# Kernel optimization log

Measured on AMD Instinct MI355X. Metric: run time of the kernel, lower is better.

The kernel has to match this reference:

```python
import jax, jax.numpy as jnp
import numpy as np

B, S, E, H = 8, 1024, 1024, 16
D = E // H  # head_dim = hidden_size // num_heads


def setup_inputs() -> dict:
    key = jax.random.key(0)
    ks = jax.random.split(key, 9)
    s = 0.02
    return {
        "h":  jax.random.normal(ks[0], (B, S, E), jnp.float32),
        # per-head projection weights stacked over heads; torch Linear(E, D) -> stored [E, D] (x @ W)
        "Wq": jax.random.normal(ks[1], (H, E, D), jnp.float32) * s,
        "bq": jax.random.normal(ks[2], (H, D), jnp.float32) * s,
        "Wk": jax.random.normal(ks[3], (H, E, D), jnp.float32) * s,
        "bk": jax.random.normal(ks[4], (H, D), jnp.float32) * s,
        "Wv": jax.random.normal(ks[5], (H, E, D), jnp.float32) * s,  # dead weight: original passes h as value
        "bv": jax.random.normal(ks[6], (H, D), jnp.float32) * s,
        "Wo": jax.random.normal(ks[7], (E, E), jnp.float32) * s,
        "bo": jax.random.normal(ks[8], (E,), jnp.float32) * s,
    }


def reference(h, Wq, bq, Wk, bk, Wv, bv, Wo, bo):
    # Batched over all heads at once instead of the original Python loop.
    q = jnp.einsum('bse,hed->bhsd', h, Wq) + bq[None, :, None, :]   # [B,H,S,D]
    k = jnp.einsum('bse,hed->bhsd', h, Wk) + bk[None, :, None, :]   # [B,H,S,D]
    # v is computed in the original module but NOT used (do_attention gets h as value)
    _v = jnp.einsum('bse,hed->bhsd', h, Wv) + bv[None, :, None, :]
    scale = 1.0 / jnp.sqrt(jnp.asarray(D, h.dtype))
    scores = jnp.einsum('bhsd,bhtd->bhst', q, k) * scale            # [B,H,S,T]
    # original: F.softmax(scores, dim=1) on per-head [B,S,T] -> query axis = axis 2 here
    weights = jax.nn.softmax(scores, axis=2)
    ctx = jnp.einsum('bhst,bte->bhse', weights, h)                  # value = h (embed_dim), per original
    # torch.cat over dim=1 of per-head [B,S,E] outputs -> [B, H*S, E]
    x = ctx.reshape(B, H * S, E)
    return x @ Wo + bo
```

## Files before the change

### kernel.cpp

```cpp
#include <hip/hip_runtime.h>

#define B_ 8
#define S_ 1024
#define E_ 1024
#define H_ 16
#define D_ 64

typedef __attribute__((ext_vector_type(8))) __bf16 bf16x8;
typedef __attribute__((ext_vector_type(4))) float f32x4;
typedef __attribute__((ext_vector_type(4))) unsigned short u16x4;
typedef __attribute__((ext_vector_type(8))) unsigned short u16x8;

static __device__ __forceinline__ unsigned short f2bf_hw(float f) {
  union { __bf16 b; unsigned short u; } v;
  v.b = (__bf16)f;
  return v.u;
}

#if __has_builtin(__builtin_amdgcn_exp2f)
#define EXP2(x) __builtin_amdgcn_exp2f(x)
#else
#define EXP2(x) exp2f(x)
#endif
#define SCALE2 0.18033688f

#define MFMA16(a, b, c) __builtin_amdgcn_mfma_f32_16x16x32_bf16((a), (b), (c), 0, 0, 0)

__global__ void cast_f32_bf16_kernel(const float* __restrict__ src,
                                     unsigned short* __restrict__ dst, int n4) {
  int i = blockIdx.x * 256 + threadIdx.x;
  if (i >= n4) return;
  float4 v = reinterpret_cast<const float4*>(src)[i];
  u16x4 o;
  o[0] = f2bf_hw(v.x); o[1] = f2bf_hw(v.y); o[2] = f2bf_hw(v.z); o[3] = f2bf_hw(v.w);
  reinterpret_cast<u16x4*>(dst)[i] = o;
}

__global__ void transpose_cast_kernel(const float* __restrict__ src,
                                      unsigned short* __restrict__ dst,
                                      int rows, int cols) {
  __shared__ unsigned short tile[64][65];
  const float* s = src + (size_t)blockIdx.z * rows * cols;
  unsigned short* d = dst + (size_t)blockIdx.z * rows * cols;
  int rb = blockIdx.y * 64, cb = blockIdx.x * 64;
#pragma unroll
  for (int k = 0; k < 16; k++) {
    int idx = threadIdx.x + 256 * k;
    int r = idx >> 6, c = idx & 63;
    tile[r][c] = f2bf_hw(s[(size_t)(rb + r) * cols + cb + c]);
  }
  __syncthreads();
#pragma unroll
  for (int k = 0; k < 16; k++) {
    int idx = threadIdx.x + 256 * k;
    int r = idx >> 6, c = idx & 63;
    d[(size_t)(cb + r) * rows + rb + c] = tile[c][r];
  }
}

__launch_bounds__(256)
__global__ void gemm_G_kernel(const unsigned short* __restrict__ hb,
                              const unsigned short* __restrict__ WoT,
                              unsigned short* __restrict__ Gt) {
  int mblk = blockIdx.x, nblk = blockIdx.y, b = blockIdx.z;
  const unsigned short* A = hb + (size_t)b * S_ * E_;
  int tid = threadIdx.x, l = tid & 63, w = tid >> 6;
  int ws = w & 1, wc = w >> 1, lr = l & 15, lg = l >> 4;
  f32x4 acc[4][4] = {};
  int ar[4], bc[4];
#pragma unroll
  for (int i = 0; i < 4; i++) ar[i] = mblk * 128 + ws * 64 + i * 16 + lr;
#pragma unroll
  for (int j = 0; j < 4; j++) bc[j] = nblk * 128 + wc * 64 + j * 16 + lr;
  for (int k0 = 0; k0 < E_; k0 += 32) {
    bf16x8 a[4], bb[4];
#pragma unroll
    for (int i = 0; i < 4; i++)
      a[i] = *reinterpret_cast<const bf16x8*>(A + (size_t)ar[i] * E_ + k0 + lg * 8);
#pragma unroll
    for (int j = 0; j < 4; j++)
      bb[j] = *reinterpret_cast<const bf16x8*>(WoT + (size_t)bc[j] * E_ + k0 + lg * 8);
#pragma unroll
    for (int i = 0; i < 4; i++)
#pragma unroll
      for (int j = 0; j < 4; j++)
        acc[i][j] = MFMA16(a[i], bb[j], acc[i][j]);
  }
#pragma unroll
  for (int i = 0; i < 4; i++) {
    int t0 = mblk * 128 + ws * 64 + i * 16 + lg * 4;
#pragma unroll
    for (int j = 0; j < 4; j++) {
      u16x4 p;
#pragma unroll
      for (int r = 0; r < 4; r++) p[r] = f2bf_hw(acc[i][j][r]);
      int e = bc[j];
      size_t addr = (((size_t)b * 4 + (e >> 8)) * 32 + (t0 >> 5)) * 8192 +
                    (size_t)(e & 255) * 32 + (t0 & 31);
      *reinterpret_cast<u16x4*>(Gt + addr) = p;
    }
  }
}

__launch_bounds__(256)
__global__ void proj_qk_kernel(const unsigned short* __restrict__ hb,
                               const unsigned short* __restrict__ WqT,
                               const unsigned short* __restrict__ WkT,
                               const float* __restrict__ bq,
                               const float* __restrict__ bk,
                               unsigned short* __restrict__ Qb,
                               unsigned short* __restrict__ Kb) {
  int sblk = blockIdx.x, z = blockIdx.y;
  int b = z >> 4, h = z & 15;
  const unsigned short* A = hb + (size_t)b * S_ * E_;
  const unsigned short* Btq = WqT + (size_t)h * D_ * E_;
  const unsigned short* Btk = WkT + (size_t)h * D_ * E_;
  int tid = threadIdx.x, l = tid & 63, w = tid >> 6;
  int ws = w & 1, wc = w >> 1, lr = l & 15, lg = l >> 4;
  f32x4 accq[4][2] = {}, acck[4][2] = {};
  int ar[4], bc[2];
#pragma unroll
  for (int i = 0; i < 4; i++) ar[i] = sblk * 128 + ws * 64 + i * 16 + lr;
#pragma unroll
  for (int j = 0; j < 2; j++) bc[j] = wc * 32 + j * 16 + lr;
  for (int k0 = 0; k0 < E_; k0 += 32) {
    bf16x8 a[4], bbq[2], bbk[2];
#pragma unroll
    for (int i = 0; i < 4; i++)
      a[i] = *reinterpret_cast<const bf16x8*>(A + (size_t)ar[i] * E_ + k0 + lg * 8);
#pragma unroll
    for (int j = 0; j < 2; j++) {
      bbq[j] = *reinterpret_cast<const bf16x8*>(Btq + (size_t)bc[j] * E_ + k0 + lg * 8);
      bbk[j] = *reinterpret_cast<const bf16x8*>(Btk + (size_t)bc[j] * E_ + k0 + lg * 8);
    }
#pragma unroll
    for (int i = 0; i < 4; i++)
#pragma unroll
      for (int j = 0; j < 2; j++) {
        accq[i][j] = MFMA16(a[i], bbq[j], accq[i][j]);
        acck[i][j] = MFMA16(a[i], bbk[j], acck[i][j]);
      }
  }
  unsigned short* oq = Qb + (size_t)z * S_ * D_;
  unsigned short* ok = Kb + (size_t)z * S_ * D_;
#pragma unroll
  for (int j = 0; j < 2; j++) {
    float bvq = bq[h * D_ + bc[j]], bvk = bk[h * D_ + bc[j]];
#pragma unroll
    for (int i = 0; i < 4; i++)
#pragma unroll
      for (int r = 0; r < 4; r++) {
        int s = sblk * 128 + ws * 64 + i * 16 + lg * 4 + r;
        oq[(size_t)s * D_ + bc[j]] = f2bf_hw(accq[i][j][r] + bvq);
        ok[(size_t)s * D_ + bc[j]] = f2bf_hw(acck[i][j][r] + bvk);
      }
  }
}

__launch_bounds__(256)
__global__ void stats_kernel(const unsigned short* __restrict__ Qb,
                             const unsigned short* __restrict__ Kb,
                             float* __restrict__ c) {
  int tblk = blockIdx.x, z = blockIdx.y;
  const unsigned short* Q = Qb + (size_t)z * S_ * D_;
  const unsigned short* K = Kb + (size_t)z * S_ * D_;
  int tid = threadIdx.x, l = tid & 63, w = tid >> 6;
  int lr = l & 15, lg = l >> 4;
  int tb = tblk * 256 + w * 64;
  const float scale = 0.125f;
  bf16x8 kb[4][2];
#pragma unroll
  for (int j = 0; j < 4; j++)
#pragma unroll
    for (int ks = 0; ks < 2; ks++)
      kb[j][ks] = *reinterpret_cast<const bf16x8*>(
          K + (size_t)(tb + j * 16 + lr) * D_ + ks * 32 + lg * 8);
  float m[4], zz[4];
#pragma unroll
  for (int j = 0; j < 4; j++) { m[j] = -1e30f; zz[j] = 0.f; }
  for (int s0 = 0; s0 < S_; s0 += 32) {
    bf16x8 aq[2][2];
#pragma unroll
    for (int sf = 0; sf < 2; sf++)
#pragma unroll
      for (int ks = 0; ks < 2; ks++)
        aq[sf][ks] = *reinterpret_cast<const bf16x8*>(
            Q + (size_t)(s0 + sf * 16 + lr) * D_ + ks * 32 + lg * 8);
    f32x4 acc[2][4] = {};
#pragma unroll
    for (int sf = 0; sf < 2; sf++)
#pragma unroll
      for (int j = 0; j < 4; j++) {
        acc[sf][j] = MFMA16(aq[sf][0], kb[j][0], acc[sf][j]);
        acc[sf][j] = MFMA16(aq[sf][1], kb[j][1], acc[sf][j]);
      }
#pragma unroll
    for (int j = 0; j < 4; j++) {
      float v[8];
#pragma unroll
      for (int sf = 0; sf < 2; sf++)
#pragma unroll
        for (int r = 0; r < 4; r++) v[sf * 4 + r] = acc[sf][j][r] * scale;
      float mx = m[j];
#pragma unroll
      for (int t = 0; t < 8; t++) mx = fmaxf(mx, v[t]);
      float sum = 0.f;
#pragma unroll
      for (int t = 0; t < 8; t++) sum += __expf(v[t] - mx);
      zz[j] = zz[j] * __expf(m[j] - mx) + sum;
      m[j] = mx;
    }
  }
#pragma unroll
  for (int j = 0; j < 4; j++) {
    float mj = m[j], zj = zz[j];
#pragma unroll
    for (int off = 16; off <= 32; off <<= 1) {
      float om = __shfl_xor(mj, off, 64);
      float oz = __shfl_xor(zj, off, 64);
      float mn = fmaxf(mj, om);
      zj = zj * __expf(mj - mn) + oz * __expf(om - mn);
      mj = mn;
    }
    if (l < 16)
      c[(size_t)z * S_ + tb + j * 16 + lr] = (mj + __logf(zj)) * 1.44269504f;
  }
}

__launch_bounds__(256, 3)
__global__ void attn_kernel(const unsigned short* __restrict__ Qb,
                            const unsigned short* __restrict__ Kb,
                            const unsigned short* __restrict__ Gt,
                            const float* __restrict__ cst,
                            const float* __restrict__ bo,
                            float* __restrict__ out) {
  int n = blockIdx.x;
  int b = n & 7, h = (n >> 3) & 15, eblk = (n >> 7) & 3, sblk = n >> 9;
  int z = b * 16 + h;
  __shared__ unsigned short Ks[2][32][72];
  __shared__ unsigned short Ps[2][64][40];
  int tid = threadIdx.x, l = tid & 63, w = tid >> 6;
  int lr = l & 15, lg = l >> 4;
  const unsigned short* Q = Qb + (size_t)z * S_ * D_ + (size_t)(sblk * 64) * D_;
  const unsigned short* K = Kb + (size_t)z * S_ * D_;
  const unsigned short* Gb = Gt + (((size_t)b * 4 + eblk) * 32) * 8192;
  const float* cz = cst + (size_t)z * S_;

  bf16x8 q[2];
#pragma unroll
  for (int ks = 0; ks < 2; ks++)
    q[ks] = *reinterpret_cast<const bf16x8*>(
        Q + (size_t)(w * 16 + lr) * D_ + ks * 32 + lg * 8);

  size_t goff[4];
#pragma unroll
  for (int j = 0; j < 4; j++)
    goff[j] = (size_t)(w * 64 + j * 16 + lr) * 32 + lg * 8;

  int krow = tid >> 3, kc8 = (tid & 7) * 8;
  u16x8 kreg;
  bf16x8 vA[4], vB[4];

  kreg = *reinterpret_cast<const u16x8*>(K + (size_t)krow * D_ + kc8);
  *reinterpret_cast<u16x8*>(&Ks[0][krow][kc8]) = kreg;
  kreg = *reinterpret_cast<const u16x8*>(K + (size_t)(32 + krow) * D_ + kc8);
#pragma unroll
  for (int j = 0; j < 4; j++)
    vA[j] = *reinterpret_cast<const bf16x8*>(Gb + goff[j]);
  __syncthreads();

  f32x4 acc[4][4] = {};

#define WINDOW(IT, CUR, VPREV, HASPV)                                             \
  do {                                                                            \
    int t0_ = (IT) * 32;                                                          \
                            \
    *reinterpret_cast<u16x8*>(&Ks[(CUR) ^ 1][krow][kc8]) = kreg;                  \
    {                                                                             \
      int tk_ = ((IT) + 2) & 31;                                                  \
      kreg = *reinterpret_cast<const u16x8*>(                                     \
          K + (size_t)(tk_ * 32 + krow) * D_ + kc8);                              \
    }                                                                             \
                                                         \
    f32x4 sa_[2] = {};                                                            \
    {                                                                             \
      bf16x8 ka_[2][2];                                                           \
      _Pragma("unroll") for (int tf = 0; tf < 2; tf++)                            \
        _Pragma("unroll") for (int ks = 0; ks < 2; ks++)                          \
          ka_[tf][ks] = *reinterpret_cast<const bf16x8*>(                         \
              &Ks[CUR][tf * 16 + lr][ks * 32 + lg * 8]);                          \
      _Pragma("unroll") for (int tf = 0; tf < 2; tf++) {                          \
        sa_[tf] = MFMA16(ka_[tf][0], q[0], sa_[tf]);                              \
        sa_[tf] = MFMA16(ka_[tf][1], q[1], sa_[tf]);                              \
      }                                                                           \
    }                                                                             \
                 \
    if (HASPV) {                                                                  \
      bf16x8 ap_[4];                                                              \
      _Pragma("unroll") for (int i = 0; i < 4; i++)                               \
        ap_[i] = *reinterpret_cast<const bf16x8*>(                                \
            &Ps[(CUR) ^ 1][i * 16 + lr][lg * 8]);                                 \
      __builtin_amdgcn_s_setprio(1);                                              \
      _Pragma("unroll") for (int i = 0; i < 4; i++)                               \
        _Pragma("unroll") for (int j = 0; j < 4; j++)                             \
          acc[i][j] = MFMA16(ap_[i], VPREV[j], acc[i][j]);                        \
      __builtin_amdgcn_s_setprio(0);                                              \
    }                                                                             \
           \
    {                                                                             \
      int tg_ = ((IT) + 1) & 31;                                                  \
      _Pragma("unroll") for (int j = 0; j < 4; j++)                               \
        VPREV[j] = *reinterpret_cast<const bf16x8*>(                              \
            Gb + (size_t)tg_ * 8192 + goff[j]);                                   \
    }                                                                             \
                                                         \
    _Pragma("unroll") for (int tf = 0; tf < 2; tf++) {                            \
      f32x4 cv_ = *reinterpret_cast<const f32x4*>(cz + t0_ + tf * 16 + lg * 4);   \
      u16x4 p_;                                                                   \
      _Pragma("unroll") for (int r = 0; r < 4; r++)                               \
        p_[r] = f2bf_hw(EXP2(fmaf(sa_[tf][r], SCALE2, -cv_[r])));                 \
      *reinterpret_cast<u16x4*>(&Ps[CUR][w * 16 + lr][tf * 16 + lg * 4]) = p_;    \
    }                                                                             \
    __syncthreads();                                                              \
  } while (0)

  for (int it2 = 0; it2 < 16; ++it2) {
    WINDOW(it2 * 2, 0, vB, (it2 > 0));
    WINDOW(it2 * 2 + 1, 1, vA, true);
  }
#undef WINDOW

  {
    bf16x8 ap_[4];
#pragma unroll
    for (int i = 0; i < 4; i++)
      ap_[i] = *reinterpret_cast<const bf16x8*>(&Ps[1][i * 16 + lr][lg * 8]);
#pragma unroll
    for (int i = 0; i < 4; i++)
#pragma unroll
      for (int j = 0; j < 4; j++)
        acc[i][j] = MFMA16(ap_[i], vB[j], acc[i][j]);
  }

  float bov[4];
#pragma unroll
  for (int j = 0; j < 4; j++) bov[j] = bo[eblk * 256 + w * 64 + j * 16 + lr];
#pragma unroll
  for (int i = 0; i < 4; i++)
#pragma unroll
    for (int j = 0; j < 4; j++)
#pragma unroll
      for (int r = 0; r < 4; r++) {
        int s = sblk * 64 + i * 16 + lg * 4 + r;
        int col = eblk * 256 + w * 64 + j * 16 + lr;
        out[((size_t)b * (H_ * S_) + (size_t)h * S_ + s) * E_ + col] =
            acc[i][j][r] + bov[j];
      }
}

extern "C" void kernel_launch(void* const* d_in, const int* in_sizes, int n_in,
                              void* d_out, int out_size, void* d_ws, size_t ws_size,
                              hipStream_t stream) {
  const float* h  = (const float*)d_in[0];
  const float* Wq = (const float*)d_in[1];
  const float* bq = (const float*)d_in[2];
  const float* Wk = (const float*)d_in[3];
  const float* bk = (const float*)d_in[4];
  const float* Wo = (const float*)d_in[7];
  const float* bo = (const float*)d_in[8];
  float* out = (float*)d_out;

  char* p = (char*)d_ws;
  unsigned short* hb  = (unsigned short*)p; p += (size_t)B_ * S_ * E_ * 2;
  unsigned short* WoT = (unsigned short*)p; p += (size_t)E_ * E_ * 2;
  unsigned short* WqT = (unsigned short*)p; p += (size_t)H_ * D_ * E_ * 2;
  unsigned short* WkT = (unsigned short*)p; p += (size_t)H_ * D_ * E_ * 2;
  unsigned short* Qb  = (unsigned short*)p; p += (size_t)B_ * H_ * S_ * D_ * 2;
  unsigned short* Kb  = (unsigned short*)p; p += (size_t)B_ * H_ * S_ * D_ * 2;
  unsigned short* Gt  = (unsigned short*)p; p += (size_t)B_ * E_ * S_ * 2;
  float*          cst = (float*)p;          p += (size_t)B_ * H_ * S_ * 4;

  int n4 = B_ * S_ * E_ / 4;
  cast_f32_bf16_kernel<<<dim3(n4 / 256), 256, 0, stream>>>(h, hb, n4);
  transpose_cast_kernel<<<dim3(16, 16, 1), 256, 0, stream>>>(Wo, WoT, E_, E_);
  transpose_cast_kernel<<<dim3(1, 16, H_), 256, 0, stream>>>(Wq, WqT, E_, D_);
  transpose_cast_kernel<<<dim3(1, 16, H_), 256, 0, stream>>>(Wk, WkT, E_, D_);
  gemm_G_kernel<<<dim3(8, 8, B_), 256, 0, stream>>>(hb, WoT, Gt);
  proj_qk_kernel<<<dim3(8, B_ * H_), 256, 0, stream>>>(hb, WqT, WkT, bq, bk, Qb, Kb);
  stats_kernel<<<dim3(S_ / 256, B_ * H_), 256, 0, stream>>>(Qb, Kb, cst);
  attn_kernel<<<dim3(8192), 256, 0, stream>>>(Qb, Kb, Gt, cst, bo, out);
}
```

Measured before the change: 645.4 us.

## Double key tile per window to 64 and stage softmax constants in LDS

Each window of the fused attention+output-projection loop now processes 64 keys instead of 32, so there are half as many windows and half as many block-wide barriers. The V/Gt prefetch is restructured to hold two 32-key slices in registers. The per-row log-sum-exp constants are loaded into shared memory once instead of being read from global memory every window. LDS use and register pressure grow (larger K/P tiles, more live V fragments), which could lower occupancy under the 3-blocks launch bound.

```diff
diff --git a/kernel.cpp b/kernel.cpp
--- a/kernel.cpp
+++ b/kernel.cpp
@@ -237,14 +237,14 @@
   int n = blockIdx.x;
   int b = n & 7, h = (n >> 3) & 15, eblk = (n >> 7) & 3, sblk = n >> 9;
   int z = b * 16 + h;
-  __shared__ unsigned short Ks[2][32][72];
-  __shared__ unsigned short Ps[2][64][40];
+  __shared__ unsigned short Ks[2][64][72];
+  __shared__ unsigned short Ps[2][64][72];
+  __shared__ float csm[1024];
   int tid = threadIdx.x, l = tid & 63, w = tid >> 6;
   int lr = l & 15, lg = l >> 4;
   const unsigned short* Q = Qb + (size_t)z * S_ * D_ + (size_t)(sblk * 64) * D_;
   const unsigned short* K = Kb + (size_t)z * S_ * D_;
   const unsigned short* Gb = Gt + (((size_t)b * 4 + eblk) * 32) * 8192;
-  const float* cz = cst + (size_t)z * S_;
 
   bf16x8 q[2];
 #pragma unroll
@@ -257,65 +257,73 @@
   for (int j = 0; j < 4; j++)
     goff[j] = (size_t)(w * 64 + j * 16 + lr) * 32 + lg * 8;
 
-  int krow = tid >> 3, kc8 = (tid & 7) * 8;
-  u16x8 kreg;
-  bf16x8 vA[4], vB[4];
-
-  kreg = *reinterpret_cast<const u16x8*>(K + (size_t)krow * D_ + kc8);
-  *reinterpret_cast<u16x8*>(&Ks[0][krow][kc8]) = kreg;
-  kreg = *reinterpret_cast<const u16x8*>(K + (size_t)(32 + krow) * D_ + kc8);
-#pragma unroll
-  for (int j = 0; j < 4; j++)
-    vA[j] = *reinterpret_cast<const bf16x8*>(Gb + goff[j]);
+  int krow = tid >> 2, kc16 = (tid & 3) * 16;
+  u16x8 kreg0, kreg1;
+  bf16x8 v[2][4];
+
+  *reinterpret_cast<f32x4*>(&csm[tid * 4]) =
+      *reinterpret_cast<const f32x4*>(cst + (size_t)z * S_ + tid * 4);
+  kreg0 = *reinterpret_cast<const u16x8*>(K + (size_t)krow * D_ + kc16);
+  kreg1 = *reinterpret_cast<const u16x8*>(K + (size_t)krow * D_ + kc16 + 8);
+  *reinterpret_cast<u16x8*>(&Ks[0][krow][kc16]) = kreg0;
+  *reinterpret_cast<u16x8*>(&Ks[0][krow][kc16 + 8]) = kreg1;
+  kreg0 = *reinterpret_cast<const u16x8*>(K + (size_t)(64 + krow) * D_ + kc16);
+  kreg1 = *reinterpret_cast<const u16x8*>(K + (size_t)(64 + krow) * D_ + kc16 + 8);
+#pragma unroll
+  for (int ks = 0; ks < 2; ks++)
+#pragma unroll
+    for (int j = 0; j < 4; j++)
+      v[ks][j] = *reinterpret_cast<const bf16x8*>(Gb + (size_t)ks * 8192 + goff[j]);
   __syncthreads();
 
   f32x4 acc[4][4] = {};
 
-#define WINDOW(IT, CUR, VPREV, HASPV)                                             \
+#define WINDOW(IT, CUR)                                                           \
   do {                                                                            \
-    int t0_ = (IT) * 32;                                                          \
+    int t0_ = (IT) * 64;                                                          \
                             \
-    *reinterpret_cast<u16x8*>(&Ks[(CUR) ^ 1][krow][kc8]) = kreg;                  \
+    *reinterpret_cast<u16x8*>(&Ks[(CUR) ^ 1][krow][kc16]) = kreg0;                \
+    *reinterpret_cast<u16x8*>(&Ks[(CUR) ^ 1][krow][kc16 + 8]) = kreg1;            \
     {                                                                             \
-      int tk_ = ((IT) + 2) & 31;                                                  \
-      kreg = *reinterpret_cast<const u16x8*>(                                     \
-          K + (size_t)(tk_ * 32 + krow) * D_ + kc8);                              \
+      int tk_ = ((IT) + 2) & 15;                                                  \
+      kreg0 = *reinterpret_cast<const u16x8*>(                                    \
+          K + (size_t)(tk_ * 64 + krow) * D_ + kc16);                             \
+      kreg1 = *reinterpret_cast<const u16x8*>(                                    \
+          K + (size_t)(tk_ * 64 + krow) * D_ + kc16 + 8);                         \
     }                                                                             \
-                                                         \
-    f32x4 sa_[2] = {};                                                            \
-    {                                                                             \
-      bf16x8 ka_[2][2];                                                           \
-      _Pragma("unroll") for (int tf = 0; tf < 2; tf++)                            \
-        _Pragma("unroll") for (int ks = 0; ks < 2; ks++)                          \
-          ka_[tf][ks] = *reinterpret_cast<const bf16x8*>(                         \
-              &Ks[CUR][tf * 16 + lr][ks * 32 + lg * 8]);                          \
-      _Pragma("unroll") for (int tf = 0; tf < 2; tf++) {                          \
-        sa_[tf] = MFMA16(ka_[tf][0], q[0], sa_[tf]);                              \
-        sa_[tf] = MFMA16(ka_[tf][1], q[1], sa_[tf]);                              \
+                                            \
+    f32x4 sa_[4];                                                                 \
+    _Pragma("unroll") for (int tf = 0; tf < 4; tf++) {                            \
+      bf16x8 ka0_ = *reinterpret_cast<const bf16x8*>(                             \
+          &Ks[CUR][tf * 16 + lr][lg * 8]);                                        \
+      bf16x8 ka1_ = *reinterpret_cast<const bf16x8*>(                             \
+          &Ks[CUR][tf * 16 + lr][32 + lg * 8]);                                   \
+      f32x4 t_ = {};                                                              \
+      t_ = MFMA16(ka0_, q[0], t_);                                                \
+      sa_[tf] = MFMA16(ka1_, q[1], t_);                                           \
+    }                                                                             \
+               \
+    if ((IT) > 0) {                                                               \
+      __builtin_amdgcn_s_setprio(1);                                              \
+      _Pragma("unroll") for (int ks = 0; ks < 2; ks++) {                          \
+        bf16x8 ap_[4];                                                            \
+        _Pragma("unroll") for (int i = 0; i < 4; i++)                             \
+          ap_[i] = *reinterpret_cast<const bf16x8*>(                              \
+              &Ps[(CUR) ^ 1][i * 16 + lr][ks * 32 + lg * 8]);                     \
+        _Pragma("unroll") for (int i = 0; i < 4; i++)                             \
+          _Pragma("unroll") for (int j = 0; j < 4; j++)                           \
+            acc[i][j] = MFMA16(ap_[i], v[ks][j], acc[i][j]);                      \
       }                                                                           \
+      __builtin_amdgcn_s_setprio(0);                                              \
+                                      \
+      _Pragma("unroll") for (int ks = 0; ks < 2; ks++)                            \
+        _Pragma("unroll") for (int j = 0; j < 4; j++)                             \
+          v[ks][j] = *reinterpret_cast<const bf16x8*>(                            \
+              Gb + ((size_t)(IT) * 2 + ks) * 8192 + goff[j]);                     \
     }                                                                             \
-                 \
-    if (HASPV) {                                                                  \
-      bf16x8 ap_[4];                                                              \
-      _Pragma("unroll") for (int i = 0; i < 4; i++)                               \
-        ap_[i] = *reinterpret_cast<const bf16x8*>(                                \
-            &Ps[(CUR) ^ 1][i * 16 + lr][lg * 8]);                                 \
-      __builtin_amdgcn_s_setprio(1);                                              \
-      _Pragma("unroll") for (int i = 0; i < 4; i++)                               \
-        _Pragma("unroll") for (int j = 0; j < 4; j++)                             \
-          acc[i][j] = MFMA16(ap_[i], VPREV[j], acc[i][j]);                        \
-      __builtin_amdgcn_s_setprio(0);                                              \
-    }                                                                             \
-           \
-    {                                                                             \
-      int tg_ = ((IT) + 1) & 31;                                                  \
-      _Pragma("unroll") for (int j = 0; j < 4; j++)                               \
-        VPREV[j] = *reinterpret_cast<const bf16x8*>(                              \
-            Gb + (size_t)tg_ * 8192 + goff[j]);                                   \
-    }                                                                             \
-                                                         \
-    _Pragma("unroll") for (int tf = 0; tf < 2; tf++) {                            \
-      f32x4 cv_ = *reinterpret_cast<const f32x4*>(cz + t0_ + tf * 16 + lg * 4);   \
+                                 \
+    _Pragma("unroll") for (int tf = 0; tf < 4; tf++) {                            \
+      f32x4 cv_ = *reinterpret_cast<const f32x4*>(&csm[t0_ + tf * 16 + lg * 4]);  \
       u16x4 p_;                                                                   \
       _Pragma("unroll") for (int r = 0; r < 4; r++)                               \
         p_[r] = f2bf_hw(EXP2(fmaf(sa_[tf][r], SCALE2, -cv_[r])));                 \
@@ -324,22 +332,25 @@
     __syncthreads();                                                              \
   } while (0)
 
-  for (int it2 = 0; it2 < 16; ++it2) {
-    WINDOW(it2 * 2, 0, vB, (it2 > 0));
-    WINDOW(it2 * 2 + 1, 1, vA, true);
+  for (int it2 = 0; it2 < 8; ++it2) {
+    WINDOW(it2 * 2, 0);
+    WINDOW(it2 * 2 + 1, 1);
   }
 #undef WINDOW
 
   {
-    bf16x8 ap_[4];
-#pragma unroll
-    for (int i = 0; i < 4; i++)
-      ap_[i] = *reinterpret_cast<const bf16x8*>(&Ps[1][i * 16 + lr][lg * 8]);
-#pragma unroll
-    for (int i = 0; i < 4; i++)
-#pragma unroll
-      for (int j = 0; j < 4; j++)
-        acc[i][j] = MFMA16(ap_[i], vB[j], acc[i][j]);
+#pragma unroll
+    for (int ks = 0; ks < 2; ks++) {
+      bf16x8 ap_[4];
+#pragma unroll
+      for (int i = 0; i < 4; i++)
+        ap_[i] = *reinterpret_cast<const bf16x8*>(&Ps[1][i * 16 + lr][ks * 32 + lg * 8]);
+#pragma unroll
+      for (int i = 0; i < 4; i++)
+#pragma unroll
+        for (int j = 0; j < 4; j++)
+          acc[i][j] = MFMA16(ap_[i], v[ks][j], acc[i][j]);
+    }
   }
 
   float bov[4];
```

Result: faster. 629.4 us, median of 2 (-2.5%).
